# Kernel tuning notes

Hardware: AMD Instinct MI355X
Metric: run time of the kernel (lower is better)

The kernel has to match this reference:

```python
import jax, jax.numpy as jnp
import numpy as np

D_IN = 1024
D_OUT = 1024

def setup_inputs() -> dict:
    key = jax.random.key(0)
    ks = jax.random.split(key, 7)
    s = 1.0 / np.sqrt(D_IN)
    x = jax.random.normal(ks[0], (4, 2048, D_IN), dtype=jnp.float32)
    Wq = jax.random.uniform(ks[1], (D_IN, D_OUT), jnp.float32, -s, s)
    bq = jax.random.uniform(ks[2], (D_OUT,), jnp.float32, -s, s)
    Wk = jax.random.uniform(ks[3], (D_IN, D_OUT), jnp.float32, -s, s)
    bk = jax.random.uniform(ks[4], (D_OUT,), jnp.float32, -s, s)
    Wv = jax.random.uniform(ks[5], (D_IN, D_OUT), jnp.float32, -s, s)
    bv = jax.random.uniform(ks[6], (D_OUT,), jnp.float32, -s, s)
    return {"x": x, "Wq": Wq, "bq": bq, "Wk": Wk, "bk": bk, "Wv": Wv, "bv": bv}

def reference(x, Wq, bq, Wk, bk, Wv, bv):
    # q,k,v: [B, T, d_out]
    q = x @ Wq + bq
    k = x @ Wk + bk
    v = x @ Wv + bv
    T = x.shape[1]
    scale = 1.0 / jnp.sqrt(jnp.asarray(D_OUT, x.dtype))
    qk = jnp.einsum('btd,bsd->bts', q, k) * scale  # [B, T, T]
    causal = jnp.tril(jnp.ones((T, T), dtype=bool))
    qk = jnp.where(causal, qk, -jnp.inf)
    probs = jax.nn.softmax(qk, axis=-1)
    return jnp.einsum('bts,bsd->btd', probs, v)
```

## Files before the change

kernel.cpp:

```cpp
#include <hip/hip_runtime.h>
#include <cstdint>
#include <cmath>

#define D_MODEL 1024
#define SEQ 2048
#define BATCH 4

typedef short bf16x8 __attribute__((ext_vector_type(8)));
typedef float f32x4 __attribute__((ext_vector_type(4)));

__device__ __forceinline__ short f2bf(float f) {
  union { float f; unsigned int u; } v; v.f = f;
  unsigned int r = (v.u + 0x7FFFu + ((v.u >> 16) & 1u)) >> 16;
  return (short)r;
}

__device__ __forceinline__ float bf2f(short h) {
  union { unsigned int u; float f; } v;
  v.u = ((unsigned int)(unsigned short)h) << 16;
  return v.f;
}

__device__ __forceinline__ f32x4 mfma16(bf16x8 a, bf16x8 b, f32x4 c) {
  return __builtin_amdgcn_mfma_f32_16x16x32_bf16(a, b, c, 0, 0, 0);
}

__device__ __forceinline__ void load_lds16(const void* g, void* l) {
  __builtin_amdgcn_global_load_lds(
      (const __attribute__((address_space(1))) unsigned int*)g,
      (__attribute__((address_space(3))) unsigned int*)l, 16, 0, 0);
}

__global__ __launch_bounds__(256) void convert_x(const float* __restrict__ x,
                                                 short* __restrict__ xb) {
  int i = blockIdx.x * 256 + threadIdx.x;
  float4 f = ((const float4*)x)[i];
  short4 h;
  h.x = f2bf(f.x); h.y = f2bf(f.y); h.z = f2bf(f.z); h.w = f2bf(f.w);
  ((short4*)xb)[i] = h;
}

__global__ __launch_bounds__(256) void transpose_w(const float* __restrict__ Wq,
                                                   const float* __restrict__ Wk,
                                                   const float* __restrict__ Wv,
                                                   short* __restrict__ wt) {
  const int mat = blockIdx.z;
  const float* __restrict__ W = (mat == 0) ? Wq : (mat == 1) ? Wk : Wv;
  short* __restrict__ o = wt + (size_t)mat * (D_MODEL * D_MODEL);
  __shared__ float tile[32][33];
  const int k0 = blockIdx.x * 32, n0 = blockIdx.y * 32;
  const int lx = threadIdx.x & 31, ly = threadIdx.x >> 5;
#pragma unroll
  for (int i = 0; i < 4; ++i) {
    int r = ly + i * 8;
    tile[r][lx] = W[(size_t)(k0 + r) * D_MODEL + n0 + lx];
  }
  __syncthreads();
#pragma unroll
  for (int i = 0; i < 4; ++i) {
    int r = ly + i * 8;
    o[(size_t)(n0 + r) * D_MODEL + k0 + lx] = f2bf(tile[lx][r]);
  }
}

__global__ __launch_bounds__(512) void qkv_gemm(
    const short* __restrict__ xb, const short* __restrict__ wt,
    const float* __restrict__ bq, const float* __restrict__ bk,
    const float* __restrict__ bv, short* __restrict__ qo,
    short* __restrict__ ko, short* __restrict__ vo) {
  const int m0 = blockIdx.x * 256;
  const int n0 = blockIdx.y * 128;
  const int mat = blockIdx.z;
  const short* __restrict__ w = wt + (size_t)mat * (D_MODEL * D_MODEL);
  const float* __restrict__ bias = (mat == 0) ? bq : (mat == 1) ? bk : bv;

  __shared__ short a_lds[2][256 * 64];
  __shared__ short b_lds[2][128 * 64];

  const int tid = threadIdx.x;
  const int wid = tid >> 6;
  const int lane = tid & 63;
  const int quad = lane >> 4;
  const int l16 = lane & 15;
  const int wm = (wid >> 1) * 64;
  const int wn = (wid & 1) * 64;
  const int sw = l16 & 7;
  const int r_local = wid * 8 + (lane >> 3);
  const int c_sw = ((lane & 7) ^ (lane >> 3)) * 8;

  f32x4 acc[4][4] = {};

  auto stage = [&](int k0, int buf) {
#pragma unroll
    for (int it = 0; it < 4; ++it)
      load_lds16(xb + (size_t)(m0 + it * 64 + r_local) * D_MODEL + k0 + c_sw,
                 (char*)a_lds[buf] + it * 8192 + wid * 1024);
#pragma unroll
    for (int it = 0; it < 2; ++it)
      load_lds16(w + (size_t)(n0 + it * 64 + r_local) * D_MODEL + k0 + c_sw,
                 (char*)b_lds[buf] + it * 8192 + wid * 1024);
  };

  stage(0, 0);
  for (int k0 = 0; k0 < D_MODEL; k0 += 64) {
    const int buf = (k0 >> 6) & 1;
    __syncthreads();
    if (k0 + 64 < D_MODEL) stage(k0 + 64, buf ^ 1);
    const short* al = a_lds[buf];
    const short* bl = b_lds[buf];
#pragma unroll
    for (int kt = 0; kt < 2; ++kt) {
      bf16x8 af[4], bfr[4];
#pragma unroll
      for (int i = 0; i < 4; ++i)
        af[i] = *(const bf16x8*)(al + (wm + i * 16 + l16) * 64 +
                                 ((kt * 4 + quad) ^ sw) * 8);
#pragma unroll
      for (int i = 0; i < 4; ++i)
        bfr[i] = *(const bf16x8*)(bl + (wn + i * 16 + l16) * 64 +
                                  ((kt * 4 + quad) ^ sw) * 8);
#pragma unroll
      for (int i = 0; i < 4; ++i)
#pragma unroll
        for (int j = 0; j < 4; ++j)
          acc[i][j] = mfma16(af[i], bfr[j], acc[i][j]);
    }
  }
#pragma unroll
  for (int i = 0; i < 4; ++i) {
#pragma unroll
    for (int j = 0; j < 4; ++j) {
#pragma unroll
      for (int r = 0; r < 4; ++r) {
        const int mrow = m0 + wm + i * 16 + quad * 4 + r;
        const int ncol = n0 + wn + j * 16 + l16;
        const float val = acc[i][j][r] + bias[ncol];
        const short h = f2bf(val);
        if (mat == 2) {
          const int bb = mrow >> 11;
          const int t = mrow & 2047;
          vo[((size_t)bb * D_MODEL + ncol) * SEQ + t] = h;
        } else if (mat == 0) {
          qo[(size_t)mrow * D_MODEL + ncol] = h;
        } else {
          ko[(size_t)mrow * D_MODEL + ncol] = h;
        }
      }
    }
  }
}

__global__ __launch_bounds__(256) void sgemm(const short* __restrict__ qb,
                                             const short* __restrict__ kb,
                                             short* __restrict__ S) {
  if (blockIdx.y > blockIdx.x) return;
  const int m0 = blockIdx.x * 128;
  const int n0 = blockIdx.y * 128;
  const int b = blockIdx.z;
  const short* __restrict__ qp = qb + (size_t)b * SEQ * D_MODEL;
  const short* __restrict__ kp = kb + (size_t)b * SEQ * D_MODEL;

  __shared__ short a_lds[2][128 * 64];
  __shared__ short b_lds[2][128 * 64];

  const int tid = threadIdx.x;
  const int wid = tid >> 6;
  const int lane = tid & 63;
  const int quad = lane >> 4;
  const int l16 = lane & 15;
  const int mw = (wid >> 1) * 64;
  const int nw = (wid & 1) * 64;
  const int sw = l16 & 7;
  const int r_local = wid * 8 + (lane >> 3);
  const int c_sw = ((lane & 7) ^ (lane >> 3)) * 8;

  f32x4 acc[4][4] = {};

  auto stage = [&](int k0, int buf) {
#pragma unroll
    for (int it = 0; it < 4; ++it) {
      load_lds16(qp + (size_t)(m0 + it * 32 + r_local) * D_MODEL + k0 + c_sw,
                 (char*)a_lds[buf] + it * 4096 + wid * 1024);
      load_lds16(kp + (size_t)(n0 + it * 32 + r_local) * D_MODEL + k0 + c_sw,
                 (char*)b_lds[buf] + it * 4096 + wid * 1024);
    }
  };

  stage(0, 0);
  for (int k0 = 0; k0 < D_MODEL; k0 += 64) {
    const int buf = (k0 >> 6) & 1;
    __syncthreads();
    if (k0 + 64 < D_MODEL) stage(k0 + 64, buf ^ 1);
    const short* al = a_lds[buf];
    const short* bl = b_lds[buf];
#pragma unroll
    for (int kt = 0; kt < 2; ++kt) {
      bf16x8 af[4], bfr[4];
#pragma unroll
      for (int i = 0; i < 4; ++i)
        af[i] = *(const bf16x8*)(al + (mw + i * 16 + l16) * 64 +
                                 ((kt * 4 + quad) ^ sw) * 8);
#pragma unroll
      for (int i = 0; i < 4; ++i)
        bfr[i] = *(const bf16x8*)(bl + (nw + i * 16 + l16) * 64 +
                                  ((kt * 4 + quad) ^ sw) * 8);
#pragma unroll
      for (int i = 0; i < 4; ++i)
#pragma unroll
        for (int j = 0; j < 4; ++j)
          acc[i][j] = mfma16(af[i], bfr[j], acc[i][j]);
    }
  }
#pragma unroll
  for (int i = 0; i < 4; ++i) {
#pragma unroll
    for (int j = 0; j < 4; ++j) {
#pragma unroll
      for (int r = 0; r < 4; ++r) {
        const int mrow = m0 + mw + i * 16 + quad * 4 + r;
        const int ncol = n0 + nw + j * 16 + l16;
        S[((size_t)b * SEQ + mrow) * SEQ + ncol] = f2bf(acc[i][j][r] * 0.03125f);
      }
    }
  }
}

__global__ __launch_bounds__(256) void softmax_rows(const short* __restrict__ S,
                                                    short* __restrict__ P) {
  const int row = blockIdx.x;
  const int t = row & (SEQ - 1);
  const int tid = threadIdx.x;
  const short* __restrict__ srow = S + (size_t)row * SEQ;
  short* __restrict__ prow = P + (size_t)row * SEQ;

  __shared__ float red[4];

  float v[8];
#pragma unroll
  for (int i = 0; i < 8; ++i) {
    const int c = tid + i * 256;
    v[i] = (c <= t) ? bf2f(srow[c]) : -1e30f;
  }
  float m = v[0];
#pragma unroll
  for (int i = 1; i < 8; ++i) m = fmaxf(m, v[i]);
#pragma unroll
  for (int o = 32; o; o >>= 1) m = fmaxf(m, __shfl_xor(m, o));
  if ((tid & 63) == 0) red[tid >> 6] = m;
  __syncthreads();
  m = fmaxf(fmaxf(red[0], red[1]), fmaxf(red[2], red[3]));

  float e[8];
  float s = 0.f;
#pragma unroll
  for (int i = 0; i < 8; ++i) {
    e[i] = __expf(v[i] - m);
    s += e[i];
  }
#pragma unroll
  for (int o = 32; o; o >>= 1) s += __shfl_xor(s, o);
  __syncthreads();
  if ((tid & 63) == 0) red[tid >> 6] = s;
  __syncthreads();
  s = red[0] + red[1] + red[2] + red[3];
  const float rinv = 1.0f / s;
  const int nwr = (t >> 8) + 1;
#pragma unroll
  for (int i = 0; i < 8; ++i)
    if (i < nwr) prow[tid + i * 256] = f2bf(e[i] * rinv);
}

__global__ __launch_bounds__(256) void pvgemm(const short* __restrict__ P,
                                              const short* __restrict__ vtb,
                                              float* __restrict__ out) {
  const int n0 = blockIdx.x * 128;
  const int b = blockIdx.y;
  const int m0 = (15 - blockIdx.z) * 128;
  const short* __restrict__ pp = P + (size_t)b * SEQ * SEQ;
  const short* __restrict__ vp = vtb + (size_t)b * D_MODEL * SEQ;
  const int kmax = m0 + 128;

  __shared__ short a_lds[2][128 * 64];
  __shared__ short b_lds[2][128 * 64];

  const int tid = threadIdx.x;
  const int wid = tid >> 6;
  const int lane = tid & 63;
  const int quad = lane >> 4;
  const int l16 = lane & 15;
  const int mw = (wid >> 1) * 64;
  const int nw = (wid & 1) * 64;
  const int sw = l16 & 7;
  const int r_local = wid * 8 + (lane >> 3);
  const int c_sw = ((lane & 7) ^ (lane >> 3)) * 8;

  f32x4 acc[4][4] = {};

  auto stage = [&](int k0, int buf) {
#pragma unroll
    for (int it = 0; it < 4; ++it) {
      load_lds16(pp + (size_t)(m0 + it * 32 + r_local) * SEQ + k0 + c_sw,
                 (char*)a_lds[buf] + it * 4096 + wid * 1024);
      load_lds16(vp + (size_t)(n0 + it * 32 + r_local) * SEQ + k0 + c_sw,
                 (char*)b_lds[buf] + it * 4096 + wid * 1024);
    }
  };

  stage(0, 0);
  for (int k0 = 0; k0 < kmax; k0 += 64) {
    const int buf = (k0 >> 6) & 1;
    __syncthreads();
    if (k0 + 64 < kmax) stage(k0 + 64, buf ^ 1);
    const short* al = a_lds[buf];
    const short* bl = b_lds[buf];
#pragma unroll
    for (int kt = 0; kt < 2; ++kt) {
      bf16x8 af[4], bfr[4];
#pragma unroll
      for (int i = 0; i < 4; ++i)
        af[i] = *(const bf16x8*)(al + (mw + i * 16 + l16) * 64 +
                                 ((kt * 4 + quad) ^ sw) * 8);
#pragma unroll
      for (int i = 0; i < 4; ++i)
        bfr[i] = *(const bf16x8*)(bl + (nw + i * 16 + l16) * 64 +
                                  ((kt * 4 + quad) ^ sw) * 8);
#pragma unroll
      for (int i = 0; i < 4; ++i)
#pragma unroll
        for (int j = 0; j < 4; ++j)
          acc[i][j] = mfma16(af[i], bfr[j], acc[i][j]);
    }
  }
#pragma unroll
  for (int i = 0; i < 4; ++i) {
#pragma unroll
    for (int j = 0; j < 4; ++j) {
#pragma unroll
      for (int r = 0; r < 4; ++r) {
        const int mrow = m0 + mw + i * 16 + quad * 4 + r;
        const int ncol = n0 + nw + j * 16 + l16;
        out[((size_t)b * SEQ + mrow) * D_MODEL + ncol] = acc[i][j][r];
      }
    }
  }
}

extern "C" void kernel_launch(void* const* d_in, const int* in_sizes, int n_in,
                              void* d_out, int out_size, void* d_ws, size_t ws_size,
                              hipStream_t stream) {
  (void)in_sizes; (void)n_in; (void)out_size; (void)ws_size;
  const float* x  = (const float*)d_in[0];
  const float* Wq = (const float*)d_in[1];
  const float* bq = (const float*)d_in[2];
  const float* Wk = (const float*)d_in[3];
  const float* bk = (const float*)d_in[4];
  const float* Wv = (const float*)d_in[5];
  const float* bv = (const float*)d_in[6];
  float* out = (float*)d_out;

  char* ws = (char*)d_ws;
  short* xb = (short*)(ws);
  short* wt = (short*)(ws + 16777216);
  short* qo = (short*)(ws + 23068672);
  short* ko = (short*)(ws + 39845888);
  short* vo = (short*)(ws + 56623104);
  short* S  = (short*)(ws + 73400320);
  short* P  = (short*)(ws);

  convert_x<<<dim3(8192), dim3(256), 0, stream>>>(x, xb);
  transpose_w<<<dim3(32, 32, 3), dim3(256), 0, stream>>>(Wq, Wk, Wv, wt);
  qkv_gemm<<<dim3(32, 8, 3), dim3(512), 0, stream>>>(xb, wt, bq, bk, bv, qo, ko, vo);
  sgemm<<<dim3(16, 16, BATCH), dim3(256), 0, stream>>>(qo, ko, S);
  softmax_rows<<<dim3(BATCH * SEQ), dim3(256), 0, stream>>>(S, P);
  pvgemm<<<dim3(8, BATCH, 16), dim3(256), 0, stream>>>(P, vo, out);
}
```

Before: 266.7 us.

## Halve QKV GEMM K-tile to 32 and raise occupancy with launch bounds

```diff
diff --git a/kernel.cpp b/kernel.cpp
--- a/kernel.cpp
+++ b/kernel.cpp
@@ -63,7 +63,7 @@
   }
 }
 
-__global__ __launch_bounds__(512) void qkv_gemm(
+__global__ __launch_bounds__(512, 4) void qkv_gemm(
     const short* __restrict__ xb, const short* __restrict__ wt,
     const float* __restrict__ bq, const float* __restrict__ bk,
     const float* __restrict__ bv, short* __restrict__ qo,
@@ -74,8 +74,8 @@
   const short* __restrict__ w = wt + (size_t)mat * (D_MODEL * D_MODEL);
   const float* __restrict__ bias = (mat == 0) ? bq : (mat == 1) ? bk : bv;
 
-  __shared__ short a_lds[2][256 * 64];
-  __shared__ short b_lds[2][128 * 64];
+  __shared__ short a_lds[2][256 * 32];
+  __shared__ short b_lds[2][128 * 32];
 
   const int tid = threadIdx.x;
   const int wid = tid >> 6;
@@ -84,47 +84,44 @@
   const int l16 = lane & 15;
   const int wm = (wid >> 1) * 64;
   const int wn = (wid & 1) * 64;
-  const int sw = l16 & 7;
-  const int r_local = wid * 8 + (lane >> 3);
-  const int c_sw = ((lane & 7) ^ (lane >> 3)) * 8;
+  const int key = (l16 >> 1) & 3;
 
   f32x4 acc[4][4] = {};
 
   auto stage = [&](int k0, int buf) {
 #pragma unroll
-    for (int it = 0; it < 4; ++it)
-      load_lds16(xb + (size_t)(m0 + it * 64 + r_local) * D_MODEL + k0 + c_sw,
-                 (char*)a_lds[buf] + it * 8192 + wid * 1024);
-#pragma unroll
-    for (int it = 0; it < 2; ++it)
-      load_lds16(w + (size_t)(n0 + it * 64 + r_local) * D_MODEL + k0 + c_sw,
-                 (char*)b_lds[buf] + it * 8192 + wid * 1024);
+    for (int h = 0; h < 2; ++h) {
+      const int c = tid + h * 512;
+      load_lds16(xb + (size_t)(m0 + (c >> 2)) * D_MODEL + k0 +
+                     (((c & 3) ^ ((c >> 3) & 3)) << 3),
+                 (char*)&a_lds[buf][c * 8]);
+    }
+    load_lds16(w + (size_t)(n0 + (tid >> 2)) * D_MODEL + k0 +
+                   (((tid & 3) ^ ((tid >> 3) & 3)) << 3),
+               (char*)&b_lds[buf][tid * 8]);
   };
 
   stage(0, 0);
-  for (int k0 = 0; k0 < D_MODEL; k0 += 64) {
-    const int buf = (k0 >> 6) & 1;
+  for (int k0 = 0; k0 < D_MODEL; k0 += 32) {
+    const int buf = (k0 >> 5) & 1;
     __syncthreads();
-    if (k0 + 64 < D_MODEL) stage(k0 + 64, buf ^ 1);
+    if (k0 + 32 < D_MODEL) stage(k0 + 32, buf ^ 1);
     const short* al = a_lds[buf];
     const short* bl = b_lds[buf];
-#pragma unroll
-    for (int kt = 0; kt < 2; ++kt) {
-      bf16x8 af[4], bfr[4];
-#pragma unroll
-      for (int i = 0; i < 4; ++i)
-        af[i] = *(const bf16x8*)(al + (wm + i * 16 + l16) * 64 +
-                                 ((kt * 4 + quad) ^ sw) * 8);
-#pragma unroll
-      for (int i = 0; i < 4; ++i)
-        bfr[i] = *(const bf16x8*)(bl + (wn + i * 16 + l16) * 64 +
-                                  ((kt * 4 + quad) ^ sw) * 8);
-#pragma unroll
-      for (int i = 0; i < 4; ++i)
-#pragma unroll
-        for (int j = 0; j < 4; ++j)
-          acc[i][j] = mfma16(af[i], bfr[j], acc[i][j]);
-    }
+    bf16x8 af[4], bfr[4];
+#pragma unroll
+    for (int i = 0; i < 4; ++i)
+      af[i] = *(const bf16x8*)(al + (wm + i * 16 + l16) * 32 +
+                               ((quad ^ key) << 3));
+#pragma unroll
+    for (int j = 0; j < 4; ++j)
+      bfr[j] = *(const bf16x8*)(bl + (wn + j * 16 + l16) * 32 +
+                                ((quad ^ key) << 3));
+#pragma unroll
+    for (int i = 0; i < 4; ++i)
+#pragma unroll
+      for (int j = 0; j < 4; ++j)
+        acc[i][j] = mfma16(af[i], bfr[j], acc[i][j]);
   }
 #pragma unroll
   for (int i = 0; i < 4; ++i) {
```

Result: no change. 263.3 us (-1.3%).
